# Optimization experiments

Measured on AMD Instinct MI355X. Metric: run time of the kernel, lower is better.

## Reference

```python
import jax, jax.numpy as jnp
import numpy as np

B, L, D_MODEL = 2, 2048, 2048
D_INNER, D_STATE, D_CONV, DT_RANK = 4096, 16, 4, 128


def setup_inputs() -> dict:
    key = jax.random.key(0)
    ks = jax.random.split(key, 8)
    s = 0.02
    return {
        "hidden_states": jax.random.normal(ks[0], (B, L, D_MODEL), jnp.float32),
        "in_proj_weight": jax.random.normal(ks[1], (2 * D_INNER, D_MODEL), jnp.float32) * s,
        "conv1d_weight": jax.random.normal(ks[2], (D_INNER, 1, D_CONV), jnp.float32) * s,
        "conv1d_bias": jnp.zeros((D_INNER,), jnp.float32),
        "x_proj_weight": jax.random.normal(ks[3], (DT_RANK + 2 * D_STATE, D_INNER), jnp.float32) * s,
        "dt_proj_weight": jax.random.normal(ks[4], (D_INNER, DT_RANK), jnp.float32) * s,
        "dt_proj_bias": jax.random.uniform(ks[5], (D_INNER,), jnp.float32, -4.0, -2.0),
        "out_proj_weight": jax.random.normal(ks[6], (D_MODEL, D_INNER), jnp.float32) * s,
        # real Mamba init: A_log = log(1..d_state) broadcast over channels
        "A_log": jnp.log(jnp.broadcast_to(jnp.arange(1, D_STATE + 1, dtype=jnp.float32), (D_INNER, D_STATE))),
        "D": jnp.ones((D_INNER,), jnp.float32),
    }


def reference(hidden_states, in_proj_weight, conv1d_weight, conv1d_bias,
              x_proj_weight, dt_proj_weight, dt_proj_bias, out_proj_weight,
              A_log, D):
    negA = -jnp.exp(A_log)  # [d_inner, d_state]
    # in_proj (no bias) then transpose(1,2): [B, 2*d_inner, L]
    xz = jnp.einsum('bld,ed->bel', hidden_states, in_proj_weight)
    x, z = jnp.split(xz, 2, axis=1)  # each [B, d_inner, L]
    # causal depthwise conv1d + silu
    x = jax.lax.conv_general_dilated(
        x, conv1d_weight, window_strides=(1,), padding=[(D_CONV - 1, 0)],
        dimension_numbers=('NCH', 'OIH', 'NCH'), feature_group_count=D_INNER,
    ) + conv1d_bias[None, :, None]
    x = jax.nn.silu(x)
    xT = x.transpose(0, 2, 1)  # [B, L, d_inner]
    # x_proj -> (dt_rank, d_state, d_state)
    x_dbl = jnp.einsum('bld,ed->ble', xT, x_proj_weight)
    dt_lo = x_dbl[..., :DT_RANK]
    Bm = x_dbl[..., DT_RANK:DT_RANK + D_STATE]   # [B, L, n]
    Cm = x_dbl[..., DT_RANK + D_STATE:]          # [B, L, n]
    # dt_proj + delta_bias, softplus (delta_softplus=True)
    dt = jax.nn.softplus(jnp.einsum('blr,dr->bld', dt_lo, dt_proj_weight) + dt_proj_bias)

    # selective scan: h_t = exp(dt_t*A)*h_{t-1} + dt_t*x_t*B_t ; y_t = C_t . h_t
    def step(h, inp):
        dt_t, B_t, C_t, x_t = inp  # [B,d],[B,n],[B,n],[B,d]
        dA = jnp.exp(dt_t[..., None] * negA)           # [B, d, n]
        h = h * dA + (dt_t * x_t)[..., None] * B_t[:, None, :]
        y = jnp.einsum('bdn,bn->bd', h, C_t)
        return h, y

    h0 = jnp.zeros((B, D_INNER, D_STATE), dt.dtype)
    _, ys = jax.lax.scan(
        step, h0,
        (dt.transpose(1, 0, 2), Bm.transpose(1, 0, 2),
         Cm.transpose(1, 0, 2), xT.transpose(1, 0, 2)),
    )  # ys: [L, B, d_inner]
    y = ys.transpose(1, 0, 2) + xT * D          # skip connection D*x
    y = y * jax.nn.silu(z.transpose(0, 2, 1))   # gate
    # out_proj (no bias): [B, L, d_model]
    return jnp.einsum('bld,ed->ble', y, out_proj_weight)
```

## Files before the change

### kernel.cpp

```cpp
#include <hip/hip_runtime.h>
#include <math.h>

#define B_ 2
#define L_ 2048
#define DMODEL 2048
#define DINNER 4096
#define DSTATE 16
#define DCONV 4
#define DTRANK 128
#define NCHUNK 32
#define CLEN 64

typedef unsigned short ushort_t;
typedef unsigned int uint_t;
typedef __attribute__((ext_vector_type(8))) short bf16x8;
typedef __attribute__((ext_vector_type(4))) float floatx4;

__device__ __forceinline__ float sigmoidf_(float x){ return 1.f/(1.f+__expf(-x)); }
__device__ __forceinline__ ushort_t f2bf(float f){
    uint_t u = __builtin_bit_cast(uint_t, f);
    return (ushort_t)((u + 0x7FFFu + ((u >> 16) & 1u)) >> 16);
}
__device__ __forceinline__ float bf2f(ushort_t h){
    return __builtin_bit_cast(float, (uint_t)h << 16);
}
__device__ __forceinline__ float fast_exp2(float x){
#if __has_builtin(__builtin_amdgcn_exp2f)
    return __builtin_amdgcn_exp2f(x);
#else
    return exp2f(x);
#endif
}
#define LOG2E 1.44269504088896f

#define GLD_LDS16(g, l) __builtin_amdgcn_global_load_lds( \
    (const __attribute__((address_space(1))) void*)(g),   \
    (__attribute__((address_space(3))) void*)(l), 16, 0, 0)

template<int OUTBF, int EPI, int NMASK, int SPLIT>
__global__ __launch_bounds__(256)
void gemm_mfma(const ushort_t* __restrict__ Aptr, int lda,
               const ushort_t* __restrict__ W, int ldw,
               void* __restrict__ Cptr, void* __restrict__ C2,
               int ldc, int K, int Nn,
               const float* __restrict__ bias)
{
    __shared__ ushort_t lsA[128*32];
    __shared__ ushort_t lsW[128*32];
    const int tid  = threadIdx.x;
    const int row0 = blockIdx.y * 128;
    const int col0 = blockIdx.x * 128;
    const int lane = tid & 63;
    const int wv   = tid >> 6;
    const int wm   = (wv >> 1) * 64;
    const int wn   = (wv & 1) * 64;
    const int lr   = lane & 15;
    const int lq   = lane >> 4;
    const int swc  = ((lq ^ (lr >> 1)) & 3) * 8;

    floatx4 acc[4][4];
    #pragma unroll
    for(int i=0;i<4;i++)
        #pragma unroll
        for(int j=0;j<4;j++)
            #pragma unroll
            for(int r=0;r<4;r++) acc[i][j][r] = 0.f;

    for(int k0 = 0; k0 < K; k0 += 32){
        #pragma unroll
        for(int it=0; it<2; it++){
            const int slot = it*256 + tid;
            const int row  = slot >> 2;
            const int seg  = (slot ^ (row >> 1)) & 3;
            const ushort_t* gw = W    + (size_t)(col0 + row)*ldw + k0 + seg*8;
            const ushort_t* ga = Aptr + (size_t)(row0 + row)*lda + k0 + seg*8;
            GLD_LDS16(gw, &lsW[slot*8]);
            GLD_LDS16(ga, &lsA[slot*8]);
        }
        __syncthreads();

        bf16x8 af[4], bw[4];
        #pragma unroll
        for(int i=0;i<4;i++){
            af[i] = *(const bf16x8*)&lsA[(wm + i*16 + lr)*32 + swc];
            bw[i] = *(const bf16x8*)&lsW[(wn + i*16 + lr)*32 + swc];
        }
        #pragma unroll
        for(int i=0;i<4;i++)
            #pragma unroll
            for(int j=0;j<4;j++)
                acc[i][j] = __builtin_amdgcn_mfma_f32_16x16x32_bf16(af[i], bw[j], acc[i][j], 0, 0, 0);
        __syncthreads();
    }

    void* dst = Cptr;
    int cbase = col0;
    if (SPLIT && col0 >= ldc){ dst = C2; cbase = col0 - ldc; }

    #pragma unroll
    for(int i=0;i<4;i++){
        #pragma unroll
        for(int r=0;r<4;r++){
            const int row = row0 + wm + i*16 + lq*4 + r;
            #pragma unroll
            for(int j=0;j<4;j++){
                const int col = cbase + wn + j*16 + lr;
                if (NMASK && col >= Nn) continue;
                float v = acc[i][j][r];
                if (EPI){
                    v += bias[col];
                    v = (v > 20.f) ? v : log1pf(expf(v));
                }
                if (OUTBF) ((ushort_t*)dst)[(size_t)row*ldc + col] = f2bf(v);
                else       ((float*)  dst)[(size_t)row*ldc + col] = v;
            }
        }
    }
}

__global__ __launch_bounds__(256)
void cvt_bf16(const float* __restrict__ in, ushort_t* __restrict__ out, int n4)
{
    const int i = blockIdx.x*256 + threadIdx.x;
    if (i < n4){
        float4 v = *(const float4*)(in + (size_t)i*4);
        union { ushort_t u[4]; uint2 q; } p;
        p.u[0]=f2bf(v.x); p.u[1]=f2bf(v.y); p.u[2]=f2bf(v.z); p.u[3]=f2bf(v.w);
        *(uint2*)(out + (size_t)i*4) = p.q;
    }
}

__global__ __launch_bounds__(256)
void cvt_pad256(const float* __restrict__ in, ushort_t* __restrict__ out)
{
    const int i = blockIdx.x*256 + threadIdx.x;
    const int row = i >> 10;
    const int c4  = i & 1023;
    union { ushort_t u[4]; uint2 q; } p;
    if (row < 160){
        float4 v = *(const float4*)(in + (size_t)row*4096 + c4*4);
        p.u[0]=f2bf(v.x); p.u[1]=f2bf(v.y); p.u[2]=f2bf(v.z); p.u[3]=f2bf(v.w);
    } else { p.u[0]=0; p.u[1]=0; p.u[2]=0; p.u[3]=0; }
    *(uint2*)(out + (size_t)i*4) = p.q;
}

__global__ __launch_bounds__(256)
void cvt_dtlo(const float* __restrict__ xdbl, ushort_t* __restrict__ out)
{
    const int i = blockIdx.x*256 + threadIdx.x;
    const int row = i >> 5;
    const int c4  = i & 31;
    float4 v = *(const float4*)(xdbl + (size_t)row*160 + c4*4);
    union { ushort_t u[4]; uint2 q; } p;
    p.u[0]=f2bf(v.x); p.u[1]=f2bf(v.y); p.u[2]=f2bf(v.z); p.u[3]=f2bf(v.w);
    *(uint2*)(out + (size_t)i*4) = p.q;
}

__global__ __launch_bounds__(256)
void conv_silu_bf(const ushort_t* __restrict__ xb, const float* __restrict__ w,
                  const float* __restrict__ bias, ushort_t* __restrict__ xc)
{
    const int gid = blockIdx.x*256 + threadIdx.x;
    const int d = gid & (DINNER-1);
    const int t = gid >> 12;
    const int l = t & (L_-1);
    float s = bias[d];
    #pragma unroll
    for(int j=0;j<DCONV;j++){
        const int ll = l - (DCONV-1) + j;
        if (ll >= 0)
            s = fmaf(bf2f(xb[(size_t)(t-(DCONV-1)+j)*DINNER + d]), w[d*DCONV+j], s);
    }
    xc[(size_t)t*DINNER + d] = f2bf(s * sigmoidf_(s));
}

__global__ __launch_bounds__(256)
void scan_phase1(const ushort_t* __restrict__ dt_bf,
                 const ushort_t* __restrict__ xconv,
                 const float* __restrict__ xdbl,
                 const float* __restrict__ A_log,
                 float* __restrict__ sc_h, float* __restrict__ sc_S)
{
    const int tid = threadIdx.x;
    const int d = blockIdx.x*256 + tid;
    const int chunk = blockIdx.y;
    const int b = blockIdx.z;
    const int l0 = chunk*CLEN;

    __shared__ float Bs[CLEN][DSTATE];
    for(int i=tid; i<CLEN*DSTATE; i+=256){
        const int row = i >> 4, n = i & 15;
        Bs[row][n] = xdbl[(size_t)(b*L_ + l0 + row)*160 + DTRANK + n];
    }
    float negA[DSTATE];
    #pragma unroll
    for(int n=0;n<DSTATE;n++) negA[n] = -expf(A_log[d*DSTATE + n]) * LOG2E;
    __syncthreads();

    float h[DSTATE], S[DSTATE];
    #pragma unroll
    for(int n=0;n<DSTATE;n++){ h[n]=0.f; S[n]=0.f; }

    size_t idx = (size_t)(b*L_ + l0)*DINNER + d;
    float dt_c = bf2f(dt_bf[idx]);
    float xv_c = bf2f(xconv[idx]);
    for(int l=0;l<CLEN;l++){
        float dt_n = 0.f, xv_n = 0.f;
        if (l+1 < CLEN){
            dt_n = bf2f(dt_bf[idx + DINNER]);
            xv_n = bf2f(xconv[idx + DINNER]);
        }
        const float dx = dt_c * xv_c;
        #pragma unroll
        for(int n=0;n<DSTATE;n++){
            const float t = dt_c * negA[n];
            S[n] += t;
            h[n] = fmaf(h[n], fast_exp2(t), dx*Bs[l][n]);
        }
        dt_c = dt_n; xv_c = xv_n;
        idx += DINNER;
    }
    const size_t o = (size_t)(b*NCHUNK + chunk)*DSTATE*DINNER + d;
    #pragma unroll
    for(int n=0;n<DSTATE;n++){
        sc_h[o + (size_t)n*DINNER] = h[n];
        sc_S[o + (size_t)n*DINNER] = S[n];
    }
}

__global__ __launch_bounds__(256)
void scan_phase2(float* __restrict__ sc_h, const float* __restrict__ sc_S)
{
    const int gid = blockIdx.x*256 + threadIdx.x;
    const int b = gid / (DSTATE*DINNER);
    const int rem = gid - b*DSTATE*DINNER;
    const size_t base = (size_t)b*NCHUNK*DSTATE*DINNER + rem;
    float H = 0.f;
    #pragma unroll
    for(int c=0;c<NCHUNK;c++){
        const size_t idx = base + (size_t)c*DSTATE*DINNER;
        const float he = sc_h[idx];
        const float S  = sc_S[idx];
        sc_h[idx] = H;
        H = fmaf(fast_exp2(S), H, he);
    }
}

__global__ __launch_bounds__(256)
void scan_phase3(const ushort_t* __restrict__ dt_bf,
                 const ushort_t* __restrict__ xconv,
                 const float* __restrict__ xdbl,
                 const ushort_t* __restrict__ z_bf,
                 const float* __restrict__ A_log,
                 const float* __restrict__ Dvec,
                 const float* __restrict__ sc_h,
                 ushort_t* __restrict__ y_bf)
{
    const int tid = threadIdx.x;
    const int d = blockIdx.x*256 + tid;
    const int chunk = blockIdx.y;
    const int b = blockIdx.z;
    const int l0 = chunk*CLEN;

    __shared__ float BCs[CLEN][2*DSTATE];
    for(int i=tid; i<CLEN*2*DSTATE; i+=256){
        const int row = i >> 5, c = i & 31;
        BCs[row][c] = xdbl[(size_t)(b*L_ + l0 + row)*160 + DTRANK + c];
    }
    float negA[DSTATE];
    #pragma unroll
    for(int n=0;n<DSTATE;n++) negA[n] = -expf(A_log[d*DSTATE + n]) * LOG2E;
    const float Dv = Dvec[d];
    float h[DSTATE];
    const size_t o = (size_t)(b*NCHUNK + chunk)*DSTATE*DINNER + d;
    #pragma unroll
    for(int n=0;n<DSTATE;n++) h[n] = sc_h[o + (size_t)n*DINNER];
    __syncthreads();

    size_t idx = (size_t)(b*L_ + l0)*DINNER + d;
    float dt_c = bf2f(dt_bf[idx]);
    float xv_c = bf2f(xconv[idx]);
    float zv_c = bf2f(z_bf[idx]);
    for(int l=0;l<CLEN;l++){
        float dt_n = 0.f, xv_n = 0.f, zv_n = 0.f;
        if (l+1 < CLEN){
            dt_n = bf2f(dt_bf[idx + DINNER]);
            xv_n = bf2f(xconv[idx + DINNER]);
            zv_n = bf2f(z_bf[idx + DINNER]);
        }
        const float dx = dt_c * xv_c;
        float y = 0.f;
        #pragma unroll
        for(int n=0;n<DSTATE;n++){
            const float t = dt_c * negA[n];
            h[n] = fmaf(h[n], fast_exp2(t), dx*BCs[l][n]);
            y = fmaf(h[n], BCs[l][DSTATE+n], y);
        }
        const float g = zv_c * sigmoidf_(zv_c);
        y_bf[idx] = f2bf(fmaf(xv_c, Dv, y) * g);
        dt_c = dt_n; xv_c = xv_n; zv_c = zv_n;
        idx += DINNER;
    }
}

extern "C" void kernel_launch(void* const* d_in, const int* in_sizes, int n_in,
                              void* d_out, int out_size, void* d_ws, size_t ws_size,
                              hipStream_t stream) {
    const float* hs      = (const float*)d_in[0];
    const float* w_in    = (const float*)d_in[1];
    const float* w_conv  = (const float*)d_in[2];
    const float* b_conv  = (const float*)d_in[3];
    const float* w_xproj = (const float*)d_in[4];
    const float* w_dt    = (const float*)d_in[5];
    const float* b_dt    = (const float*)d_in[6];
    const float* w_out   = (const float*)d_in[7];
    const float* A_log   = (const float*)d_in[8];
    const float* Dvec    = (const float*)d_in[9];
    float* out = (float*)d_out;

    char* base = (char*)d_ws;
    ushort_t* x_bf   = (ushort_t*)(base);
    float*    xdbl   = (float*)   (base);
    ushort_t* wx_bf  = (ushort_t*)(base + (4u<<20));
    ushort_t* dtlo_bf= (ushort_t*)(base + (6u<<20));
    ushort_t* wdt_bf = (ushort_t*)(base + (7u<<20));
    float*    sc_h   = (float*)   (base + (8u<<20));
    ushort_t* z_bf   = (ushort_t*)(base + (32u<<20));
    ushort_t* xconv  = (ushort_t*)(base + (64u<<20));
    ushort_t* wi_bf  = (ushort_t*)(base + (96u<<20));
    ushort_t* dt_bf  = (ushort_t*)(base + (96u<<20));
    ushort_t* hs_bf  = (ushort_t*)(base + (128u<<20));
    float*    sc_S   = (float*)   (base + (128u<<20));
    ushort_t* wo_bf  = (ushort_t*)(base + (128u<<20));
    ushort_t* y_bf   = (ushort_t*)(base + (144u<<20));

    const int M = B_*L_;
    dim3 blk(256);

    cvt_bf16<<<dim3(M*DMODEL/4/256), blk, 0, stream>>>(hs, hs_bf, M*DMODEL/4);
    cvt_bf16<<<dim3(2*DINNER*DMODEL/4/256), blk, 0, stream>>>(w_in, wi_bf, 2*DINNER*DMODEL/4);

    gemm_mfma<1,0,0,1><<<dim3(2*DINNER/128, M/128), blk, 0, stream>>>(
        hs_bf, DMODEL, wi_bf, DMODEL, x_bf, z_bf, DINNER, DMODEL, DINNER, nullptr);

    conv_silu_bf<<<dim3((size_t)M*DINNER/256), blk, 0, stream>>>(x_bf, w_conv, b_conv, xconv);

    cvt_pad256<<<dim3(256*4096/4/256), blk, 0, stream>>>(w_xproj, wx_bf);
    gemm_mfma<0,0,1,0><<<dim3(2, M/128), blk, 0, stream>>>(
        xconv, DINNER, wx_bf, DINNER, xdbl, nullptr, 160, DINNER, 160, nullptr);

    cvt_dtlo<<<dim3(M*32/256), blk, 0, stream>>>(xdbl, dtlo_bf);
    cvt_bf16<<<dim3(DINNER*DTRANK/4/256), blk, 0, stream>>>(w_dt, wdt_bf, DINNER*DTRANK/4);
    gemm_mfma<1,1,0,0><<<dim3(DINNER/128, M/128), blk, 0, stream>>>(
        dtlo_bf, DTRANK, wdt_bf, DTRANK, dt_bf, nullptr, DINNER, DTRANK, DINNER, b_dt);

    dim3 sgrid(DINNER/256, NCHUNK, B_);
    scan_phase1<<<sgrid, blk, 0, stream>>>(dt_bf, xconv, xdbl, A_log, sc_h, sc_S);
    scan_phase2<<<dim3(B_*DSTATE*DINNER/256), blk, 0, stream>>>(sc_h, sc_S);

    cvt_bf16<<<dim3(DMODEL*DINNER/4/256), blk, 0, stream>>>(w_out, wo_bf, DMODEL*DINNER/4);

    scan_phase3<<<sgrid, blk, 0, stream>>>(dt_bf, xconv, xdbl, z_bf, A_log, Dvec, sc_h, y_bf);

    gemm_mfma<0,0,0,0><<<dim3(DMODEL/128, M/128), blk, 0, stream>>>(
        y_bf, DINNER, wo_bf, DINNER, out, nullptr, DMODEL, DINNER, DMODEL, nullptr);
}
```

Measured before the change: 802.6 us.

## Deepen GEMM K-tile to 64, swap grid axes, split-K the x_proj GEMM

The GEMM kernel now stages 64-wide K slices per barrier with an 8-way XOR swizzle, doing two MFMA sub-steps per load, which halves the number of synchronisation rounds. The grid is transposed so consecutive blocks walk M with a fixed weight tile, changing cache locality. The narrow x_proj GEMM, which previously launched only 64 blocks, is split 8 ways over K into partial buffers, and a new reduction kernel sums them and also emits the bf16 dt_lo operand, replacing the separate conversion. The costs are more LDS per block (possibly lower occupancy), extra partial-sum memory traffic, and one more kernel launch.

```diff
diff --git a/kernel.cpp b/kernel.cpp
--- a/kernel.cpp
+++ b/kernel.cpp
@@ -10,6 +10,7 @@
 #define DTRANK 128
 #define NCHUNK 32
 #define CLEN 64
+#define MROWS 4096
 
 typedef unsigned short ushort_t;
 typedef unsigned int uint_t;
@@ -37,26 +38,26 @@
     (const __attribute__((address_space(1))) void*)(g),   \
     (__attribute__((address_space(3))) void*)(l), 16, 0, 0)
 
-template<int OUTBF, int EPI, int NMASK, int SPLIT>
+template<int OUTBF, int EPI, int SPLIT, int KSPLIT>
 __global__ __launch_bounds__(256)
 void gemm_mfma(const ushort_t* __restrict__ Aptr, int lda,
                const ushort_t* __restrict__ W, int ldw,
                void* __restrict__ Cptr, void* __restrict__ C2,
-               int ldc, int K, int Nn,
+               int ldc, int Klen,
                const float* __restrict__ bias)
 {
-    __shared__ ushort_t lsA[128*32];
-    __shared__ ushort_t lsW[128*32];
+    __shared__ ushort_t lsA[128*64];
+    __shared__ ushort_t lsW[128*64];
     const int tid  = threadIdx.x;
-    const int row0 = blockIdx.y * 128;
-    const int col0 = blockIdx.x * 128;
+    const int row0 = blockIdx.x * 128;
+    const int col0 = blockIdx.y * 128;
+    const int koff = KSPLIT ? blockIdx.z * Klen : 0;
     const int lane = tid & 63;
     const int wv   = tid >> 6;
     const int wm   = (wv >> 1) * 64;
     const int wn   = (wv & 1) * 64;
     const int lr   = lane & 15;
     const int lq   = lane >> 4;
-    const int swc  = ((lq ^ (lr >> 1)) & 3) * 8;
 
     floatx4 acc[4][4];
     #pragma unroll
@@ -66,36 +67,43 @@
             #pragma unroll
             for(int r=0;r<4;r++) acc[i][j][r] = 0.f;
 
-    for(int k0 = 0; k0 < K; k0 += 32){
-        #pragma unroll
-        for(int it=0; it<2; it++){
+    for(int k0 = koff; k0 < koff + Klen; k0 += 64){
+        #pragma unroll
+        for(int it=0; it<4; it++){
             const int slot = it*256 + tid;
-            const int row  = slot >> 2;
-            const int seg  = (slot ^ (row >> 1)) & 3;
-            const ushort_t* gw = W    + (size_t)(col0 + row)*ldw + k0 + seg*8;
-            const ushort_t* ga = Aptr + (size_t)(row0 + row)*lda + k0 + seg*8;
+            const int row  = slot >> 3;
+            const int p    = slot & 7;
+            const int s    = p ^ (row & 7);
+            const ushort_t* gw = W    + (size_t)(col0 + row)*ldw + k0 + s*8;
+            const ushort_t* ga = Aptr + (size_t)(row0 + row)*lda + k0 + s*8;
             GLD_LDS16(gw, &lsW[slot*8]);
             GLD_LDS16(ga, &lsA[slot*8]);
         }
         __syncthreads();
 
-        bf16x8 af[4], bw[4];
-        #pragma unroll
-        for(int i=0;i<4;i++){
-            af[i] = *(const bf16x8*)&lsA[(wm + i*16 + lr)*32 + swc];
-            bw[i] = *(const bf16x8*)&lsW[(wn + i*16 + lr)*32 + swc];
-        }
-        #pragma unroll
-        for(int i=0;i<4;i++)
+        #pragma unroll
+        for(int kk=0; kk<2; kk++){
+            bf16x8 af[4], bw[4];
             #pragma unroll
-            for(int j=0;j<4;j++)
-                acc[i][j] = __builtin_amdgcn_mfma_f32_16x16x32_bf16(af[i], bw[j], acc[i][j], 0, 0, 0);
+            for(int i=0;i<4;i++){
+                const int ra = wm + i*16 + lr;
+                const int rb = wn + i*16 + lr;
+                af[i] = *(const bf16x8*)&lsA[ra*64 + (((kk*4+lq) ^ (ra&7))*8)];
+                bw[i] = *(const bf16x8*)&lsW[rb*64 + (((kk*4+lq) ^ (rb&7))*8)];
+            }
+            #pragma unroll
+            for(int i=0;i<4;i++)
+                #pragma unroll
+                for(int j=0;j<4;j++)
+                    acc[i][j] = __builtin_amdgcn_mfma_f32_16x16x32_bf16(af[i], bw[j], acc[i][j], 0, 0, 0);
+        }
         __syncthreads();
     }
 
     void* dst = Cptr;
     int cbase = col0;
     if (SPLIT && col0 >= ldc){ dst = C2; cbase = col0 - ldc; }
+    const size_t zoff = KSPLIT ? (size_t)blockIdx.z * MROWS * ldc : 0;
 
     #pragma unroll
     for(int i=0;i<4;i++){
@@ -105,14 +113,13 @@
             #pragma unroll
             for(int j=0;j<4;j++){
                 const int col = cbase + wn + j*16 + lr;
-                if (NMASK && col >= Nn) continue;
                 float v = acc[i][j][r];
                 if (EPI){
                     v += bias[col];
                     v = (v > 20.f) ? v : log1pf(expf(v));
                 }
                 if (OUTBF) ((ushort_t*)dst)[(size_t)row*ldc + col] = f2bf(v);
-                else       ((float*)  dst)[(size_t)row*ldc + col] = v;
+                else       ((float*)  dst)[zoff + (size_t)row*ldc + col] = v;
             }
         }
     }
@@ -145,15 +152,17 @@
 }
 
 __global__ __launch_bounds__(256)
-void cvt_dtlo(const float* __restrict__ xdbl, ushort_t* __restrict__ out)
-{
-    const int i = blockIdx.x*256 + threadIdx.x;
-    const int row = i >> 5;
-    const int c4  = i & 31;
-    float4 v = *(const float4*)(xdbl + (size_t)row*160 + c4*4);
-    union { ushort_t u[4]; uint2 q; } p;
-    p.u[0]=f2bf(v.x); p.u[1]=f2bf(v.y); p.u[2]=f2bf(v.z); p.u[3]=f2bf(v.w);
-    *(uint2*)(out + (size_t)i*4) = p.q;
+void reduce_xproj(const float* __restrict__ P, float* __restrict__ xdbl,
+                  ushort_t* __restrict__ dtlo)
+{
+    const int row = blockIdx.x;
+    const int col = threadIdx.x;
+    float s = 0.f;
+    #pragma unroll
+    for(int z=0; z<8; z++)
+        s += P[(size_t)z*MROWS*256 + (size_t)row*256 + col];
+    if (col < 160) xdbl[(size_t)row*160 + col] = s;
+    if (col < DTRANK) dtlo[(size_t)row*DTRANK + col] = f2bf(s);
 }
 
 __global__ __launch_bounds__(256)
@@ -332,27 +341,27 @@
     ushort_t* hs_bf  = (ushort_t*)(base + (128u<<20));
     float*    sc_S   = (float*)   (base + (128u<<20));
     ushort_t* wo_bf  = (ushort_t*)(base + (128u<<20));
+    float*    xp_par = (float*)   (base + (144u<<20));
     ushort_t* y_bf   = (ushort_t*)(base + (144u<<20));
 
-    const int M = B_*L_;
     dim3 blk(256);
 
-    cvt_bf16<<<dim3(M*DMODEL/4/256), blk, 0, stream>>>(hs, hs_bf, M*DMODEL/4);
+    cvt_bf16<<<dim3(MROWS*DMODEL/4/256), blk, 0, stream>>>(hs, hs_bf, MROWS*DMODEL/4);
     cvt_bf16<<<dim3(2*DINNER*DMODEL/4/256), blk, 0, stream>>>(w_in, wi_bf, 2*DINNER*DMODEL/4);
 
-    gemm_mfma<1,0,0,1><<<dim3(2*DINNER/128, M/128), blk, 0, stream>>>(
-        hs_bf, DMODEL, wi_bf, DMODEL, x_bf, z_bf, DINNER, DMODEL, DINNER, nullptr);
-
-    conv_silu_bf<<<dim3((size_t)M*DINNER/256), blk, 0, stream>>>(x_bf, w_conv, b_conv, xconv);
+    gemm_mfma<1,0,1,0><<<dim3(MROWS/128, 2*DINNER/128), blk, 0, stream>>>(
+        hs_bf, DMODEL, wi_bf, DMODEL, x_bf, z_bf, DINNER, DMODEL, nullptr);
+
+    conv_silu_bf<<<dim3((size_t)MROWS*DINNER/256), blk, 0, stream>>>(x_bf, w_conv, b_conv, xconv);
 
     cvt_pad256<<<dim3(256*4096/4/256), blk, 0, stream>>>(w_xproj, wx_bf);
-    gemm_mfma<0,0,1,0><<<dim3(2, M/128), blk, 0, stream>>>(
-        xconv, DINNER, wx_bf, DINNER, xdbl, nullptr, 160, DINNER, 160, nullptr);
-
-    cvt_dtlo<<<dim3(M*32/256), blk, 0, stream>>>(xdbl, dtlo_bf);
+    gemm_mfma<0,0,0,1><<<dim3(MROWS/128, 2, 8), blk, 0, stream>>>(
+        xconv, DINNER, wx_bf, DINNER, xp_par, nullptr, 256, DINNER/8, nullptr);
+    reduce_xproj<<<dim3(MROWS), blk, 0, stream>>>(xp_par, xdbl, dtlo_bf);
+
     cvt_bf16<<<dim3(DINNER*DTRANK/4/256), blk, 0, stream>>>(w_dt, wdt_bf, DINNER*DTRANK/4);
-    gemm_mfma<1,1,0,0><<<dim3(DINNER/128, M/128), blk, 0, stream>>>(
-        dtlo_bf, DTRANK, wdt_bf, DTRANK, dt_bf, nullptr, DINNER, DTRANK, DINNER, b_dt);
+    gemm_mfma<1,1,0,0><<<dim3(MROWS/128, DINNER/128), blk, 0, stream>>>(
+        dtlo_bf, DTRANK, wdt_bf, DTRANK, dt_bf, nullptr, DINNER, DTRANK, b_dt);
 
     dim3 sgrid(DINNER/256, NCHUNK, B_);
     scan_phase1<<<sgrid, blk, 0, stream>>>(dt_bf, xconv, xdbl, A_log, sc_h, sc_S);
@@ -362,6 +371,6 @@
 
     scan_phase3<<<sgrid, blk, 0, stream>>>(dt_bf, xconv, xdbl, z_bf, A_log, Dvec, sc_h, y_bf);
 
-    gemm_mfma<0,0,0,0><<<dim3(DMODEL/128, M/128), blk, 0, stream>>>(
-        y_bf, DINNER, wo_bf, DINNER, out, nullptr, DMODEL, DINNER, DMODEL, nullptr);
-}
+    gemm_mfma<0,0,0,0><<<dim3(MROWS/128, DMODEL/128), blk, 0, stream>>>(
+        y_bf, DINNER, wo_bf, DINNER, out, nullptr, DMODEL, DINNER, nullptr);
+}
```

Result: faster. 685.4 us (-14.6%).
